# Kernel tuning notes

Measured on AMD Instinct MI355X. Metric: run time of the kernel, lower is better.

Reference implementation:

```python
import jax, jax.numpy as jnp
import numpy as np

N_NODES = 100000
N_EDGES = 1600000
D_IN, D_HID, D_LAT = 128, 128, 64


def setup_inputs() -> dict:
    key = jax.random.key(0)
    ks = jax.random.split(key, 8)
    x = jax.random.normal(ks[0], (N_NODES, D_IN), dtype=jnp.float32)
    edge_index = jax.random.randint(ks[1], (2, N_EDGES), 0, N_NODES, dtype=jnp.int64)
    s1 = 1.0 / np.sqrt(D_IN)
    s2 = 1.0 / np.sqrt(D_HID)
    return {
        "x": x,
        "edge_index": edge_index,
        "W1_l": jax.random.normal(ks[2], (D_IN, D_HID), dtype=jnp.float32) * s1,
        "W1_r": jax.random.normal(ks[3], (D_IN, D_HID), dtype=jnp.float32) * s1,
        "b1": jnp.zeros((D_HID,), dtype=jnp.float32),
        "W2_l": jax.random.normal(ks[4], (D_HID, D_LAT), dtype=jnp.float32) * s2,
        "W2_r": jax.random.normal(ks[5], (D_HID, D_LAT), dtype=jnp.float32) * s2,
        "b2": jnp.zeros((D_LAT,), dtype=jnp.float32),
    }


def _sage_conv_mean(x, src, dst, W_l, W_r, b):
    """PyG SAGEConv with mean aggregation: lin_l(mean_j x_j) + lin_r(x_i)."""
    n = x.shape[0]
    # scatter-mean of source features into destination nodes
    agg = jax.ops.segment_sum(x[src], dst, num_segments=n)           # [N, d]
    deg = jax.ops.segment_sum(jnp.ones_like(dst, dtype=x.dtype), dst, num_segments=n)
    mean = agg / jnp.maximum(deg, 1.0)[:, None]
    return mean @ W_l + b + x @ W_r


def reference(x, edge_index, W1_l, W1_r, b1, W2_l, W2_r, b2):
    src, dst = edge_index[0], edge_index[1]
    h = jax.nn.relu(_sage_conv_mean(x, src, dst, W1_l, W1_r, b1))
    # Dropout(p=0.2) is identity in eval mode
    z = jax.nn.relu(_sage_conv_mean(h, src, dst, W2_l, W2_r, b2))
    return z
```

## Files before the change

kernel.cpp:

```cpp
#include <hip/hip_runtime.h>

#define N_NODES 100000
#define N_EDGES 1600000
#define D_IN 128
#define D_HID 128
#define D_LAT 64

#define BSHIFT 8
#define NB 392
#define CAP 4608
#define EPB 4096
#define PART_BLOCKS ((N_EDGES + EPB - 1) / EPB)
#define CVT_BLOCKS (((long)N_NODES * 128 / 16 + 255) / 256)
#define PK1_BASE PART_BLOCKS
#define PK2L_BASE (PK1_BASE + 16)
#define PK2R_BASE (PK2L_BASE + 4)
#define CVT_BASE (PK2R_BASE + 4)

typedef unsigned short ushort_t;
typedef unsigned int uint_t;
typedef unsigned char uchar_t;
using bf16x8 = __attribute__((ext_vector_type(8))) short;
using f32x4  = __attribute__((ext_vector_type(4))) float;
using f32x2  = __attribute__((ext_vector_type(2))) float;

__device__ inline ushort_t f2bf(float f) {
    uint_t u = __float_as_uint(f);
    return (ushort_t)((u + 0x7fffu + ((u >> 16) & 1u)) >> 16);
}
__device__ inline uint_t pack2bf(float a, float b) {
    return (uint_t)f2bf(a) | ((uint_t)f2bf(b) << 16);
}
__device__ inline float bf2f(ushort_t u) {
    return __uint_as_float(((uint_t)u) << 16);
}

#if __has_builtin(__builtin_amdgcn_cvt_pk_f32_fp8) && __has_builtin(__builtin_amdgcn_cvt_pk_fp8_f32)
#define HW_FP8 1
template<bool HI>
__device__ inline f32x2 fp8pk2f(uint_t v) {
    return __builtin_amdgcn_cvt_pk_f32_fp8(v, HI);
}
__device__ inline uint_t f2fp8pk4(float a, float b, float c, float d) {
    uint_t w = __builtin_amdgcn_cvt_pk_fp8_f32(a, b, 0, false);
    w = __builtin_amdgcn_cvt_pk_fp8_f32(c, d, w, true);
    return w;
}
__device__ inline uchar_t f2fp8_byte(float f) {
    return (uchar_t)(__builtin_amdgcn_cvt_pk_fp8_f32(f, f, 0, false) & 0xff);
}
#else
__device__ inline float fp8b2f(uint_t b) {
    uint_t em = b & 0x7f;
    if (em == 0) return 0.f;
    uint_t bits = ((em << 20) + (120u << 23)) | ((b & 0x80u) << 24);
    return __uint_as_float(bits);
}
template<bool HI>
__device__ inline f32x2 fp8pk2f(uint_t v) {
    uint_t w = HI ? (v >> 16) : v;
    f32x2 r; r.x = fp8b2f(w & 0xff); r.y = fp8b2f((w >> 8) & 0xff);
    return r;
}
__device__ inline uint_t f2fp8_1(float f) {
    uint_t u = __float_as_uint(f);
    uint_t s = (u >> 31) << 7;
    uint_t au = u & 0x7fffffff;
    if (au >= 0x43e00000u) return s | 0x7e;
    if (au < 0x3c000000u) return s;
    uint_t r = au + 0x0007ffffu + ((au >> 20) & 1u);
    return s | (((r >> 20) - (120u << 3)) & 0x7f);
}
__device__ inline uint_t f2fp8pk4(float a, float b, float c, float d) {
    return f2fp8_1(a) | (f2fp8_1(b) << 8) | (f2fp8_1(c) << 16) | (f2fp8_1(d) << 24);
}
__device__ inline uchar_t f2fp8_byte(float f) { return (uchar_t)f2fp8_1(f); }
#endif

__device__ inline void accf8x4p(f32x2* a, uint_t w, int b2) {
    a[b2]     += fp8pk2f<false>(w);
    a[b2 + 1] += fp8pk2f<true>(w);
}
__device__ inline void accf8x16p(f32x2* a, uint4 u) {
    accf8x4p(a, u.x, 0); accf8x4p(a, u.y, 2); accf8x4p(a, u.z, 4); accf8x4p(a, u.w, 6);
}

template<int RSHIFT, int NV, int STRIDE, int D>
__device__ inline void gather_tail_step(const uchar_t* __restrict__ base,
                                        const int* __restrict__ idxp,
                                        int n, int& k, f32x2* acc) {
    if (k + D <= n) {
        int idt[D];
        #pragma unroll
        for (int j = 0; j < D; ++j) idt[j] = idxp[(k + j) * STRIDE];
        uint4 u[D][NV];
        #pragma unroll
        for (int j = 0; j < D; ++j) {
            #pragma unroll
            for (int v = 0; v < NV; ++v)
                u[j][v] = *(const uint4*)(base + ((long)idt[j] << RSHIFT) + v * 16);
        }
        #pragma unroll
        for (int j = 0; j < D; ++j) {
            #pragma unroll
            for (int v = 0; v < NV; ++v)
                accf8x16p(acc + v * 8, u[j][v]);
        }
        k += D;
    }
}

template<int RSHIFT, int NV, int DEPTH, int STRIDE = 1>
__device__ inline void gather_acc_fp8n(const uchar_t* __restrict__ base,
                                       const int* __restrict__ idxp,
                                       int n, f32x2* acc) {
    int k = 0;
    int idx[DEPTH];
    if (n >= DEPTH) {
        #pragma unroll
        for (int j = 0; j < DEPTH; ++j) idx[j] = idxp[j * STRIDE];
    }
    while (k + DEPTH <= n) {
        uint4 u[DEPTH][NV];
        #pragma unroll
        for (int j = 0; j < DEPTH; ++j) {
            #pragma unroll
            for (int v = 0; v < NV; ++v)
                u[j][v] = *(const uint4*)(base + ((long)idx[j] << RSHIFT) + v * 16);
        }
        int kn = k + DEPTH;
        if (kn + DEPTH <= n) {
            #pragma unroll
            for (int j = 0; j < DEPTH; ++j) idx[j] = idxp[(kn + j) * STRIDE];
        }
        #pragma unroll
        for (int j = 0; j < DEPTH; ++j) {
            #pragma unroll
            for (int v = 0; v < NV; ++v)
                accf8x16p(acc + v * 8, u[j][v]);
        }
        k = kn;
    }
    gather_tail_step<RSHIFT, NV, STRIDE, 4>(base, idxp, n, k, acc);
    gather_tail_step<RSHIFT, NV, STRIDE, 2>(base, idxp, n, k, acc);
    gather_tail_step<RSHIFT, NV, STRIDE, 1>(base, idxp, n, k, acc);
}

__device__ inline void pack_w256(const float* Wl, const float* Wr, ushort_t* pack,
                                 int N, int tid) {
    int lane = tid & 63;
    int t = tid >> 6;
    int kt = t & 7;
    int nt = t >> 3;
    int n = nt * 16 + (lane & 15);
    int kbase = kt * 32 + (lane >> 4) * 8;
    ushort_t v[8];
    #pragma unroll
    for (int j = 0; j < 8; ++j) {
        int k = kbase + j;
        float w = (k < 128) ? Wl[k * N + n] : Wr[(k - 128) * N + n];
        v[j] = f2bf(w);
    }
    *(uint4*)(pack + (long)tid * 8) = *(uint4*)v;
}
__device__ inline void pack_w128(const float* W, ushort_t* pack, int N, int tid) {
    int lane = tid & 63;
    int t = tid >> 6;
    int kt = t & 3;
    int nt = t >> 2;
    int n = nt * 16 + (lane & 15);
    int kbase = kt * 32 + (lane >> 4) * 8;
    ushort_t v[8];
    #pragma unroll
    for (int j = 0; j < 8; ++j) v[j] = f2bf(W[(kbase + j) * N + n]);
    *(uint4*)(pack + (long)tid * 8) = *(uint4*)v;
}

__global__ __launch_bounds__(256) void prep_kernel(
        const int* __restrict__ src, const int* __restrict__ dst,
        int* __restrict__ gCurRel, int* __restrict__ bedges,
        const float* __restrict__ W1_l, const float* __restrict__ W1_r,
        ushort_t* __restrict__ pack1,
        const float* __restrict__ W2_l, ushort_t* __restrict__ pack2l,
        const float* __restrict__ W2_r, ushort_t* __restrict__ pack2r,
        const float* __restrict__ x, ushort_t* __restrict__ xb,
        uchar_t* __restrict__ x8) {
    int b = blockIdx.x;
    if (b < PART_BLOCKS) {
        __shared__ int h[NB];
        __shared__ int start[NB];
        for (int j = threadIdx.x; j < NB; j += 256) h[j] = 0;
        __syncthreads();
        long base = (long)b * EPB + threadIdx.x * 16;
        int dc[16], sc[16];
        int cnt = 0;
        if (base + 16 <= N_EDGES) {
            #pragma unroll
            for (int j = 0; j < 4; ++j) {
                int4 d4 = *(const int4*)(dst + base + j * 4);
                int4 s4 = *(const int4*)(src + base + j * 4);
                dc[j * 4 + 0] = d4.x; dc[j * 4 + 1] = d4.y; dc[j * 4 + 2] = d4.z; dc[j * 4 + 3] = d4.w;
                sc[j * 4 + 0] = s4.x; sc[j * 4 + 1] = s4.y; sc[j * 4 + 2] = s4.z; sc[j * 4 + 3] = s4.w;
            }
            cnt = 16;
        } else if (base < N_EDGES) {
            cnt = (int)(N_EDGES - base);
            for (int j = 0; j < cnt; ++j) { dc[j] = dst[base + j]; sc[j] = src[base + j]; }
        }
        for (int j = 0; j < cnt; ++j) atomicAdd(&h[dc[j] >> BSHIFT], 1);
        __syncthreads();
        for (int j = threadIdx.x; j < NB; j += 256)
            start[j] = h[j] ? (j * CAP + atomicAdd(&gCurRel[j], h[j])) : 0;
        __syncthreads();
        for (int j = 0; j < cnt; ++j) {
            int bk = dc[j] >> BSHIFT;
            int p = atomicAdd(&start[bk], 1);
            if (p < (bk + 1) * CAP)
                bedges[p] = ((dc[j] & 255) << 24) | sc[j];
        }
    } else if (b < PK2L_BASE) {
        pack_w256(W1_l, W1_r, pack1, 128, (b - PK1_BASE) * 256 + threadIdx.x);
    } else if (b < PK2R_BASE) {
        pack_w128(W2_l, pack2l, 64, (b - PK2L_BASE) * 256 + threadIdx.x);
    } else if (b < CVT_BASE) {
        pack_w128(W2_r, pack2r, 64, (b - PK2R_BASE) * 256 + threadIdx.x);
    } else {
        long i = ((long)(b - CVT_BASE) * 256 + threadIdx.x) * 16;
        if (i >= (long)N_NODES * 128) return;
        float4 a = *(const float4*)(x + i);
        float4 bb = *(const float4*)(x + i + 4);
        float4 c = *(const float4*)(x + i + 8);
        float4 d = *(const float4*)(x + i + 12);
        uint4 ob0, ob1;
        ob0.x = pack2bf(a.x, a.y);  ob0.y = pack2bf(a.z, a.w);
        ob0.z = pack2bf(bb.x, bb.y); ob0.w = pack2bf(bb.z, bb.w);
        ob1.x = pack2bf(c.x, c.y);  ob1.y = pack2bf(c.z, c.w);
        ob1.z = pack2bf(d.x, d.y);  ob1.w = pack2bf(d.z, d.w);
        *(uint4*)(xb + i) = ob0;
        *(uint4*)(xb + i + 8) = ob1;
        uint4 o8;
        o8.x = f2fp8pk4(a.x, a.y, a.z, a.w);
        o8.y = f2fp8pk4(bb.x, bb.y, bb.z, bb.w);
        o8.z = f2fp8pk4(c.x, c.y, c.z, c.w);
        o8.w = f2fp8pk4(d.x, d.y, d.z, d.w);
        *(uint4*)(x8 + i) = o8;
    }
}

__global__ __launch_bounds__(256) void bucket_sort_kernel(const int* __restrict__ gCurRel,
                                                          const int* __restrict__ bedges,
                                                          int* __restrict__ csr,
                                                          int2* __restrict__ off2) {
    __shared__ int sdata[256];
    __shared__ int cur[256];
    int b = blockIdx.x, t = threadIdx.x;
    int r0 = b * CAP;
    int n = gCurRel[b];
    if (n > CAP) n = CAP;
    cur[t] = 0;
    __syncthreads();
    for (int k = t * 4; k < n; k += 1024) {
        int4 v4 = *(const int4*)(bedges + r0 + k);
        int m = n - k;
        atomicAdd(&cur[(unsigned)v4.x >> 24], 1);
        if (m > 1) atomicAdd(&cur[(unsigned)v4.y >> 24], 1);
        if (m > 2) atomicAdd(&cur[(unsigned)v4.z >> 24], 1);
        if (m > 3) atomicAdd(&cur[(unsigned)v4.w >> 24], 1);
    }
    __syncthreads();
    int c = cur[t];
    sdata[t] = c;
    __syncthreads();
    for (int d = 1; d < 256; d <<= 1) {
        int u = (t >= d) ? sdata[t - d] : 0;
        __syncthreads();
        sdata[t] += u;
        __syncthreads();
    }
    int ex = (t == 0) ? 0 : sdata[t - 1];
    off2[(b << BSHIFT) + t] = make_int2(r0 + ex, c);
    cur[t] = ex;
    __syncthreads();
    for (int k = t * 4; k < n; k += 1024) {
        int4 v4 = *(const int4*)(bedges + r0 + k);
        int m = n - k;
        {
            int p = atomicAdd(&cur[(unsigned)v4.x >> 24], 1);
            csr[r0 + p] = v4.x & 0xFFFFFF;
        }
        if (m > 1) {
            int p = atomicAdd(&cur[(unsigned)v4.y >> 24], 1);
            csr[r0 + p] = v4.y & 0xFFFFFF;
        }
        if (m > 2) {
            int p = atomicAdd(&cur[(unsigned)v4.z >> 24], 1);
            csr[r0 + p] = v4.z & 0xFFFFFF;
        }
        if (m > 3) {
            int p = atomicAdd(&cur[(unsigned)v4.w >> 24], 1);
            csr[r0 + p] = v4.w & 0xFFFFFF;
        }
    }
}

#define HSTRIDE 132
__global__ __launch_bounds__(256) void mfma_mlp_fused_kernel(
        const int2* __restrict__ off2, const int* __restrict__ csr_src,
        const uchar_t* __restrict__ x8,
        const ushort_t* __restrict__ Ax,
        const ushort_t* __restrict__ pack1, const float* __restrict__ bias,
        const ushort_t* __restrict__ pack2l, const ushort_t* __restrict__ pack2r,
        ushort_t* __restrict__ f2, uchar_t* __restrict__ g8) {
    __shared__ ushort_t mtile[32 * HSTRIDE];
    __shared__ ushort_t htile[32 * HSTRIDE];
    long m0b = (long)blockIdx.x * 32;
    {
        int lane8 = threadIdx.x & 7;
        int local = threadIdx.x >> 3;
        long i = m0b + local;
        int2 bd = off2[i];
        const uchar_t* gbase = x8 + lane8 * 16;
        f32x2 acc2[8];
        #pragma unroll
        for (int j = 0; j < 8; ++j) acc2[j] = (f32x2){0.f, 0.f};
        gather_acc_fp8n<7, 1, 8, 1>(gbase, csr_src + bd.x, bd.y, acc2);
        float* pa = (float*)acc2;
        float inv = (bd.y > 0) ? 1.f / (float)bd.y : 0.f;
        uint4 o0, o1;
        o0.x = pack2bf(pa[0] * inv,  pa[1] * inv);
        o0.y = pack2bf(pa[2] * inv,  pa[3] * inv);
        o0.z = pack2bf(pa[4] * inv,  pa[5] * inv);
        o0.w = pack2bf(pa[6] * inv,  pa[7] * inv);
        o1.x = pack2bf(pa[8] * inv,  pa[9] * inv);
        o1.y = pack2bf(pa[10] * inv, pa[11] * inv);
        o1.z = pack2bf(pa[12] * inv, pa[13] * inv);
        o1.w = pack2bf(pa[14] * inv, pa[15] * inv);
        ushort_t* mp = mtile + local * HSTRIDE + lane8 * 16;
        *(uint4*)mp = o0;
        *(uint4*)(mp + 8) = o1;
    }
    __syncthreads();
    int lane = threadIdx.x & 63;
    int wave = threadIdx.x >> 6;
    int wr = wave & 1;
    int wc = wave >> 1;
    int r = lane & 15;
    int quad = lane >> 4;
    int rowl = wr * 16 + r;
    long arow = m0b + rowl;

    bf16x8 areg[8];
    #pragma unroll
    for (int kt = 0; kt < 8; ++kt) {
        int k = (kt & 3) * 32 + quad * 8;
        areg[kt] = (kt < 4)
            ? *(const bf16x8*)(&mtile[rowl * HSTRIDE + k])
            : *(const bf16x8*)(Ax + arow * 128 + k);
    }

    f32x4 acc[4];
    #pragma unroll
    for (int nt = 0; nt < 4; ++nt) acc[nt] = (f32x4){0.f, 0.f, 0.f, 0.f};
    #pragma unroll
    for (int nt = 0; nt < 4; ++nt) {
        int gnt = wc * 4 + nt;
        #pragma unroll
        for (int kt = 0; kt < 8; ++kt) {
            bf16x8 bfrag = *(const bf16x8*)(pack1 + ((long)(gnt * 8 + kt) * 64 + lane) * 8);
            acc[nt] = __builtin_amdgcn_mfma_f32_16x16x32_bf16(areg[kt], bfrag, acc[nt], 0, 0, 0);
        }
    }

    #pragma unroll
    for (int nt = 0; nt < 4; ++nt) {
        int col = wc * 64 + nt * 16 + r;
        float bj = bias[col];
        #pragma unroll
        for (int q = 0; q < 4; ++q) {
            float v = fmaxf(acc[nt][q] + bj, 0.f);
            htile[(wr * 16 + quad * 4 + q) * HSTRIDE + col] = f2bf(v);
        }
    }
    __syncthreads();
    bf16x8 areg2[4];
    #pragma unroll
    for (int kt = 0; kt < 4; ++kt)
        areg2[kt] = *(const bf16x8*)(&htile[rowl * HSTRIDE + kt * 32 + quad * 8]);
    f32x4 gacc[2];
    #pragma unroll
    for (int nt = 0; nt < 2; ++nt) gacc[nt] = (f32x4){0.f, 0.f, 0.f, 0.f};
    #pragma unroll
    for (int nt = 0; nt < 2; ++nt) {
        int gnt = wc * 2 + nt;
        #pragma unroll
        for (int kt = 0; kt < 4; ++kt) {
            bf16x8 bfrag = *(const bf16x8*)(pack2l + ((long)(gnt * 4 + kt) * 64 + lane) * 8);
            gacc[nt] = __builtin_amdgcn_mfma_f32_16x16x32_bf16(areg2[kt], bfrag, gacc[nt], 0, 0, 0);
        }
    }
    #pragma unroll
    for (int nt = 0; nt < 2; ++nt) {
        int col = wc * 32 + nt * 16 + r;
        #pragma unroll
        for (int q = 0; q < 4; ++q) {
            long orow = m0b + wr * 16 + quad * 4 + q;
            g8[orow * 64 + col] = f2fp8_byte(gacc[nt][q]);
        }
    }
    f32x4 facc[2];
    #pragma unroll
    for (int nt = 0; nt < 2; ++nt) facc[nt] = (f32x4){0.f, 0.f, 0.f, 0.f};
    #pragma unroll
    for (int nt = 0; nt < 2; ++nt) {
        int gnt = wc * 2 + nt;
        #pragma unroll
        for (int kt = 0; kt < 4; ++kt) {
            bf16x8 bfrag = *(const bf16x8*)(pack2r + ((long)(gnt * 4 + kt) * 64 + lane) * 8);
            facc[nt] = __builtin_amdgcn_mfma_f32_16x16x32_bf16(areg2[kt], bfrag, facc[nt], 0, 0, 0);
        }
    }
    #pragma unroll
    for (int nt = 0; nt < 2; ++nt) {
        int col = wc * 32 + nt * 16 + r;
        #pragma unroll
        for (int q = 0; q < 4; ++q) {
            long orow = m0b + wr * 16 + quad * 4 + q;
            f2[orow * 64 + col] = f2bf(facc[nt][q]);
        }
    }
}

__global__ __launch_bounds__(256) void final_gather_kernel(
        const int2* __restrict__ off2, const int* __restrict__ csr_src,
        const uchar_t* __restrict__ g8,
        const ushort_t* __restrict__ f2, const float* __restrict__ b2,
        float* __restrict__ out) {
    int lane8 = threadIdx.x & 7;
    int d = lane8 & 3;
    int p = lane8 >> 2;
    int local = threadIdx.x >> 3;
    long i = (long)blockIdx.x * 32 + local;
    int2 bd = off2[i];
    int n = bd.y;
    int dim0 = d * 16 + p * 8;
    ushort_t fu[8];
    *(uint4*)fu = *(const uint4*)(f2 + i * 64 + dim0);
    float4 bj0 = *(const float4*)(b2 + dim0);
    float4 bj1 = *(const float4*)(b2 + dim0 + 4);
    const uchar_t* base = g8 + d * 16;
    f32x2 acc2[8];
    #pragma unroll
    for (int j = 0; j < 8; ++j) acc2[j] = (f32x2){0.f, 0.f};
    int np = (n + 1 - p) >> 1;
    gather_acc_fp8n<6, 1, 8, 2>(base, csr_src + bd.x + p, np, acc2);
    float* pa = (float*)acc2;
    #pragma unroll
    for (int j = 0; j < 16; ++j) pa[j] += __shfl_xor(pa[j], 4);
    float inv = (n > 0) ? 1.f / (float)n : 0.f;
    float bja[8] = {bj0.x, bj0.y, bj0.z, bj0.w, bj1.x, bj1.y, bj1.z, bj1.w};
    float o[8];
    #pragma unroll
    for (int j = 0; j < 8; ++j) {
        float m = bf2f(f2bf(pa[p * 8 + j] * inv));
        o[j] = fmaxf(m + bf2f(fu[j]) + bja[j], 0.f);
    }
    *(float4*)(out + i * 64 + dim0)     = make_float4(o[0], o[1], o[2], o[3]);
    *(float4*)(out + i * 64 + dim0 + 4) = make_float4(o[4], o[5], o[6], o[7]);
}

extern "C" void kernel_launch(void* const* d_in, const int* in_sizes, int n_in,
                              void* d_out, int out_size, void* d_ws, size_t ws_size,
                              hipStream_t stream) {
    const float* x    = (const float*)d_in[0];
    const int*   ei   = (const int*)d_in[1];
    const float* W1_l = (const float*)d_in[2];
    const float* W1_r = (const float*)d_in[3];
    const float* b1   = (const float*)d_in[4];
    const float* W2_l = (const float*)d_in[5];
    const float* W2_r = (const float*)d_in[6];
    const float* b2   = (const float*)d_in[7];
    float* out = (float*)d_out;

    const int* src = ei;
    const int* dst = ei + N_EDGES;

    int*  gCur   = (int*)d_ws;
    int2* off2   = (int2*)(gCur + 512);
    int*  bedges = (int*)(off2 + 100608);
    int*  csr    = bedges + NB * CAP;
    ushort_t* xb = (ushort_t*)(csr + NB * CAP);
    uchar_t*  x8 = (uchar_t*)(xb + (long)N_NODES * 128);
    ushort_t* f2 = (ushort_t*)(x8 + (long)N_NODES * 128);
    ushort_t* pack1  = f2 + (long)N_NODES * 64;
    ushort_t* pack2l = pack1 + 256 * 128;
    ushort_t* pack2r = pack2l + 128 * 64;
    uchar_t*  g8     = (uchar_t*)(pack2r + 128 * 64);

    hipMemsetAsync(gCur, 0, NB * sizeof(int), stream);
    prep_kernel<<<CVT_BASE + CVT_BLOCKS, 256, 0, stream>>>(
        src, dst, gCur, bedges,
        W1_l, W1_r, pack1, W2_l, pack2l, W2_r, pack2r, x, xb, x8);

    bucket_sort_kernel<<<NB, 256, 0, stream>>>(gCur, bedges, csr, off2);

    mfma_mlp_fused_kernel<<<N_NODES / 32, 256, 0, stream>>>(
        off2, csr, x8, xb, pack1, b1, pack2l, pack2r, f2, g8);

    final_gather_kernel<<<N_NODES / 32, 256, 0, stream>>>(
        off2, csr, g8, f2, b2, out);
}
```

Measured before the change: 224.1 us.

## Process nodes in degree-sorted order to balance gather work across waves

Builds a histogram of node in-degrees during the bucket sort. A new kernel then uses a counting sort to produce a permutation of nodes in descending degree order. The fused MLP kernel and the final gather kernel walk nodes through this permutation, so nodes of similar degree share a wave and per-lane gather loop lengths match more closely. The cost is an extra kernel launch, contended global atomics on a few histogram bins, and indirect row addressing for Ax reads and f2/g8/out writes, which lose contiguity across rows.

```diff
diff --git a/kernel.cpp b/kernel.cpp
--- a/kernel.cpp
+++ b/kernel.cpp
@@ -250,7 +250,8 @@
 __global__ __launch_bounds__(256) void bucket_sort_kernel(const int* __restrict__ gCurRel,
                                                           const int* __restrict__ bedges,
                                                           int* __restrict__ csr,
-                                                          int2* __restrict__ off2) {
+                                                          int2* __restrict__ off2,
+                                                          int* __restrict__ dhist) {
     __shared__ int sdata[256];
     __shared__ int cur[256];
     int b = blockIdx.x, t = threadIdx.x;
@@ -269,6 +270,7 @@
     }
     __syncthreads();
     int c = cur[t];
+    atomicAdd(&dhist[c > 255 ? 255 : c], 1);
     sdata[t] = c;
     __syncthreads();
     for (int d = 1; d < 256; d <<= 1) {
@@ -303,8 +305,32 @@
     }
 }
 
+__global__ __launch_bounds__(256) void perm_scatter_kernel(
+        const int2* __restrict__ off2, const int* __restrict__ dhist,
+        int* __restrict__ dcur, int* __restrict__ perm) {
+    __shared__ int sdata[256];
+    int t = threadIdx.x;
+    sdata[t] = dhist[255 - t];
+    __syncthreads();
+    for (int d = 1; d < 256; d <<= 1) {
+        int u = (t >= d) ? sdata[t - d] : 0;
+        __syncthreads();
+        sdata[t] += u;
+        __syncthreads();
+    }
+    int i = blockIdx.x * 256 + t;
+    if (i < N_NODES) {
+        int deg = off2[i].y; if (deg > 255) deg = 255;
+        int j = 255 - deg;
+        int basej = (j == 0) ? 0 : sdata[j - 1];
+        int pos = basej + atomicAdd(&dcur[deg], 1);
+        perm[pos] = i;
+    }
+}
+
 #define HSTRIDE 132
 __global__ __launch_bounds__(256) void mfma_mlp_fused_kernel(
+        const int* __restrict__ perm,
         const int2* __restrict__ off2, const int* __restrict__ csr_src,
         const uchar_t* __restrict__ x8,
         const ushort_t* __restrict__ Ax,
@@ -313,12 +339,14 @@
         ushort_t* __restrict__ f2, uchar_t* __restrict__ g8) {
     __shared__ ushort_t mtile[32 * HSTRIDE];
     __shared__ ushort_t htile[32 * HSTRIDE];
-    long m0b = (long)blockIdx.x * 32;
+    __shared__ int nids[32];
+    int m0b = blockIdx.x * 32;
     {
         int lane8 = threadIdx.x & 7;
         int local = threadIdx.x >> 3;
-        long i = m0b + local;
-        int2 bd = off2[i];
+        int nid = perm[m0b + local];
+        if (lane8 == 0) nids[local] = nid;
+        int2 bd = off2[nid];
         const uchar_t* gbase = x8 + lane8 * 16;
         f32x2 acc2[8];
         #pragma unroll
@@ -347,7 +375,7 @@
     int r = lane & 15;
     int quad = lane >> 4;
     int rowl = wr * 16 + r;
-    long arow = m0b + rowl;
+    long arow = nids[rowl];
 
     bf16x8 areg[8];
     #pragma unroll
@@ -403,7 +431,7 @@
         int col = wc * 32 + nt * 16 + r;
         #pragma unroll
         for (int q = 0; q < 4; ++q) {
-            long orow = m0b + wr * 16 + quad * 4 + q;
+            long orow = nids[wr * 16 + quad * 4 + q];
             g8[orow * 64 + col] = f2fp8_byte(gacc[nt][q]);
         }
     }
@@ -424,13 +452,14 @@
         int col = wc * 32 + nt * 16 + r;
         #pragma unroll
         for (int q = 0; q < 4; ++q) {
-            long orow = m0b + wr * 16 + quad * 4 + q;
+            long orow = nids[wr * 16 + quad * 4 + q];
             f2[orow * 64 + col] = f2bf(facc[nt][q]);
         }
     }
 }
 
 __global__ __launch_bounds__(256) void final_gather_kernel(
+        const int* __restrict__ perm,
         const int2* __restrict__ off2, const int* __restrict__ csr_src,
         const uchar_t* __restrict__ g8,
         const ushort_t* __restrict__ f2, const float* __restrict__ b2,
@@ -439,7 +468,7 @@
     int d = lane8 & 3;
     int p = lane8 >> 2;
     int local = threadIdx.x >> 3;
-    long i = (long)blockIdx.x * 32 + local;
+    long i = perm[blockIdx.x * 32 + local];
     int2 bd = off2[i];
     int n = bd.y;
     int dim0 = d * 16 + p * 8;
@@ -485,7 +514,10 @@
     const int* dst = ei + N_EDGES;
 
     int*  gCur   = (int*)d_ws;
-    int2* off2   = (int2*)(gCur + 512);
+    int*  dhist  = gCur + 512;
+    int*  dcur   = dhist + 256;
+    int*  perm   = dcur + 256;
+    int2* off2   = (int2*)(perm + 100352);
     int*  bedges = (int*)(off2 + 100608);
     int*  csr    = bedges + NB * CAP;
     ushort_t* xb = (ushort_t*)(csr + NB * CAP);
@@ -496,16 +528,19 @@
     ushort_t* pack2r = pack2l + 128 * 64;
     uchar_t*  g8     = (uchar_t*)(pack2r + 128 * 64);
 
-    hipMemsetAsync(gCur, 0, NB * sizeof(int), stream);
+    hipMemsetAsync(gCur, 0, (512 + 256 + 256) * sizeof(int), stream);
     prep_kernel<<<CVT_BASE + CVT_BLOCKS, 256, 0, stream>>>(
         src, dst, gCur, bedges,
         W1_l, W1_r, pack1, W2_l, pack2l, W2_r, pack2r, x, xb, x8);
 
-    bucket_sort_kernel<<<NB, 256, 0, stream>>>(gCur, bedges, csr, off2);
+    bucket_sort_kernel<<<NB, 256, 0, stream>>>(gCur, bedges, csr, off2, dhist);
+
+    perm_scatter_kernel<<<(N_NODES + 255) / 256, 256, 0, stream>>>(
+        off2, dhist, dcur, perm);
 
     mfma_mlp_fused_kernel<<<N_NODES / 32, 256, 0, stream>>>(
-        off2, csr, x8, xb, pack1, b1, pack2l, pack2r, f2, g8);
+        perm, off2, csr, x8, xb, pack1, b1, pack2l, pack2r, f2, g8);
 
     final_gather_kernel<<<N_NODES / 32, 256, 0, stream>>>(
-        off2, csr, g8, f2, b2, out);
-}
+        perm, off2, csr, g8, f2, b2, out);
+}
```

Result: slower. 741.1 us (+230.7%).
